# Optimization experiments

Measured on AMD Instinct MI355X. Metric: run time of the kernel, lower is better.

The kernel has to match this reference:

```python
import jax, jax.numpy as jnp
import numpy as np

N, E, FDIM, HID, HEADS, C, L, G = 50000, 800000, 512, 256, 8, 32, 3, 64
EPS = 1e-5


def setup_inputs() -> dict:
    key = jax.random.key(0)
    ks = jax.random.split(key, 16)
    x = jax.random.normal(ks[0], (N, FDIM), dtype=jnp.float32)
    edge_index = jax.random.randint(ks[1], (2, E), 0, N, dtype=jnp.int32)
    batch = jnp.sort(jax.random.randint(ks[2], (N,), 0, G, dtype=jnp.int32))
    s = lambda f: 1.0 / np.sqrt(f)
    return {
        "x": x,
        "edge_index": edge_index,
        "batch": batch,
        "in_w": jax.random.normal(ks[3], (FDIM, HID), jnp.float32) * s(FDIM),
        "in_b": jnp.zeros((HID,), jnp.float32),
        "gat_w": jax.random.normal(ks[4], (L, HID, HID), jnp.float32) * s(HID),
        "att_src": jax.random.normal(ks[5], (L, HEADS, C), jnp.float32) * s(C),
        "att_dst": jax.random.normal(ks[6], (L, HEADS, C), jnp.float32) * s(C),
        "gat_b": jnp.zeros((L, HID), jnp.float32),
        "res_w": jax.random.normal(ks[7], (L, HID, HID), jnp.float32) * s(HID),
        "res_b": jnp.zeros((L, HID), jnp.float32),
        "ln_g": jnp.ones((L, HID), jnp.float32),
        "ln_b": jnp.zeros((L, HID), jnp.float32),
        "pool_w": jax.random.normal(ks[8], (2 * HID, HID), jnp.float32) * s(2 * HID),
        "pool_b": jnp.zeros((HID,), jnp.float32),
    }


def _gat_layer(h, src, dst, w, a_src, a_dst, b):
    # PyG GATConv, concat=True, negative_slope=0.2, dropout inactive (eval)
    xh = (h @ w).reshape(N, HEADS, C)                      # [N,H,C]
    asn = jnp.einsum('nhc,hc->nh', xh, a_src)              # [N,H]
    adn = jnp.einsum('nhc,hc->nh', xh, a_dst)
    e = jax.nn.leaky_relu(asn[src] + adn[dst], 0.2)        # [E2,H]
    # scatter-softmax over destination neighborhoods
    m = jax.ops.segment_max(e, dst, num_segments=N)
    m = jnp.where(jnp.isfinite(m), m, 0.0)
    ex = jnp.exp(e - m[dst])
    den = jax.ops.segment_sum(ex, dst, num_segments=N)
    alpha = ex / (den[dst] + 1e-16)                        # [E2,H]
    msg = xh[src] * alpha[:, :, None]                      # [E2,H,C]
    out = jax.ops.segment_sum(msg, dst, num_segments=N)    # [N,H,C]
    return out.reshape(N, HID) + b


def _layer_norm(h, g, b):
    mu = jnp.mean(h, axis=-1, keepdims=True)
    var = jnp.mean((h - mu) ** 2, axis=-1, keepdims=True)
    return (h - mu) * jax.lax.rsqrt(var + EPS) * g + b


def reference(x, edge_index, batch, in_w, in_b, gat_w, att_src, att_dst, gat_b,
              res_w, res_b, ln_g, ln_b, pool_w, pool_b):
    loops = jnp.arange(N, dtype=edge_index.dtype)          # GATConv add_self_loops=True
    src = jnp.concatenate([edge_index[0], loops])
    dst = jnp.concatenate([edge_index[1], loops])
    h = x @ in_w + in_b
    for i in range(L):
        h_res = h @ res_w[i] + res_b[i]
        h = _gat_layer(h, src, dst, gat_w[i], att_src[i], att_dst[i], gat_b[i])
        h = jax.nn.relu(_layer_norm(h + h_res, ln_g[i], ln_b[i]))
    ones = jnp.ones((N,), h.dtype)
    cnt = jax.ops.segment_sum(ones, batch, num_segments=G)
    h_mean = jax.ops.segment_sum(h, batch, num_segments=G) / jnp.maximum(cnt, 1.0)[:, None]
    h_max = jax.ops.segment_max(h, batch, num_segments=G)
    h_cat = jnp.concatenate([h_mean, h_max], axis=1)       # [G, 2*HID]
    return jax.nn.relu(h_cat @ pool_w + pool_b)            # [G, HID]
```

## Files before the change

kernel.cpp:

```cpp
#include <hip/hip_runtime.h>
#include <math.h>

#define N_NODES 50000
#define E_EDGES 800000
#define E2 (E_EDGES + N_NODES)
#define M_PAD 50048
#define FDIM 512
#define HID 256
#define HEADS 8
#define CDIM 32
#define LAYERS 3
#define GRAPHS 64
#define LN_EPS 1e-5f
#define POOL_P 16

typedef unsigned short ushort_t;
typedef __attribute__((ext_vector_type(8))) short short8v;
typedef __attribute__((ext_vector_type(4))) float f32x4;

__device__ __forceinline__ float bf2f(ushort_t u) {
    union { unsigned int i; float f; } v;
    v.i = ((unsigned int)u) << 16;
    return v.f;
}
__device__ __forceinline__ ushort_t f2bf(float f) {
    union { float f; unsigned int u; } v;
    v.f = f;
    unsigned int r = (v.u + 0x7FFFu + ((v.u >> 16) & 1u)) >> 16;
    return (ushort_t)r;
}
__device__ __forceinline__ void gload_lds16(const void* g, void* l) {
    __builtin_amdgcn_global_load_lds(
        (const __attribute__((address_space(1))) void*)g,
        (__attribute__((address_space(3))) void*)l, 16, 0, 0);
}

__global__ void k_count(const int* __restrict__ ei, int* __restrict__ cnt) {
    int e = blockIdx.x * 256 + threadIdx.x;
    if (e >= E2) return;
    int dst = (e < E_EDGES) ? ei[E_EDGES + e] : (e - E_EDGES);
    atomicAdd(&cnt[dst], 1);
}

__global__ void k_scan1(const int* __restrict__ cnt, int* __restrict__ part) {
    __shared__ int s[256];
    int t = threadIdx.x;
    int i = blockIdx.x * 256 + t;
    s[t] = (i < N_NODES) ? cnt[i] : 0;
    __syncthreads();
    for (int d = 128; d > 0; d >>= 1) {
        if (t < d) s[t] += s[t + d];
        __syncthreads();
    }
    if (t == 0) part[blockIdx.x] = s[0];
}

__global__ void k_scan2(int* __restrict__ part, int nb, int* __restrict__ rowptr) {
    __shared__ int s[256];
    int t = threadIdx.x;
    int v = (t < nb) ? part[t] : 0;
    s[t] = v;
    __syncthreads();
    for (int d = 1; d < 256; d <<= 1) {
        int x = (t >= d) ? s[t - d] : 0;
        __syncthreads();
        s[t] += x;
        __syncthreads();
    }
    if (t < nb) part[t] = s[t] - v;
    if (t == 255) rowptr[N_NODES] = s[255];
}

__global__ void k_scan3(const int* __restrict__ cnt, const int* __restrict__ part,
                        int* __restrict__ rowptr) {
    __shared__ int s[256];
    int t = threadIdx.x;
    int i = blockIdx.x * 256 + t;
    int v = (i < N_NODES) ? cnt[i] : 0;
    s[t] = v;
    __syncthreads();
    for (int d = 1; d < 256; d <<= 1) {
        int x = (t >= d) ? s[t - d] : 0;
        __syncthreads();
        s[t] += x;
        __syncthreads();
    }
    if (i < N_NODES) rowptr[i] = part[blockIdx.x] + s[t] - v;
}

__global__ void k_fill(const int* __restrict__ ei, const int* __restrict__ rowptr,
                       int* __restrict__ fill, int* __restrict__ colv) {
    int e = blockIdx.x * 256 + threadIdx.x;
    if (e >= E2) return;
    int src, dst;
    if (e < E_EDGES) { src = ei[e]; dst = ei[E_EDGES + e]; }
    else             { src = dst = e - E_EDGES; }
    int pos = atomicAdd(&fill[dst], 1);
    colv[rowptr[dst] + pos] = src;
}

__global__ void k_bounds(const int* __restrict__ batch, int* __restrict__ rowstart) {
    int n = blockIdx.x * 256 + threadIdx.x;
    if (n >= N_NODES) return;
    int b = batch[n];
    int bp = (n == 0) ? -1 : batch[n - 1];
    for (int g = bp + 1; g <= b; ++g) rowstart[g] = n;
    if (n == N_NODES - 1) {
        for (int g = b + 1; g <= GRAPHS; ++g) rowstart[g] = N_NODES;
    }
}

__global__ __launch_bounds__(256) void k_cast_x(const float* __restrict__ x,
                                                ushort_t* __restrict__ xb) {
    long long i8 = ((long long)blockIdx.x * 256 + threadIdx.x) * 8;
    if (i8 >= (long long)M_PAD * FDIM) return;
    int row = (int)(i8 >> 9);
    ushort_t o[8];
    if (row < N_NODES) {
        const float* p = x + i8;
        #pragma unroll
        for (int j = 0; j < 8; ++j) o[j] = f2bf(p[j]);
    } else {
        #pragma unroll
        for (int j = 0; j < 8; ++j) o[j] = 0;
    }
    *(short8v*)(xb + i8) = *(short8v*)o;
}

#define MAT_ELEMS (HID * HID)
#define WT_TOTAL (2 * LAYERS * MAT_ELEMS)
__global__ __launch_bounds__(256) void k_wtrans_all(const float* __restrict__ gat_w,
                                                    const float* __restrict__ res_w,
                                                    ushort_t* __restrict__ wt2) {
    int r = blockIdx.x * 256 + threadIdx.x;
    if (r >= WT_TOTAL) return;
    int mat = r >> 16;
    int layer = mat >> 1;
    int isgat = mat & 1;
    int within = r & 65535;
    int k = within >> 8, n = within & 255;
    const float* W = (isgat ? gat_w : res_w) + (size_t)layer * MAT_ELEMS;
    wt2[(size_t)layer * 512 * HID + (size_t)(isgat * 256 + n) * HID + k] =
        f2bf(W[within]);
}

__global__ __launch_bounds__(256) void k_wcomb(const float* __restrict__ in_w,
                                               const ushort_t* __restrict__ wt2_0,
                                               const float* __restrict__ in_b,
                                               const float* __restrict__ res_w0,
                                               const float* __restrict__ gat_w0,
                                               const float* __restrict__ res_b0,
                                               ushort_t* __restrict__ wtC,
                                               float* __restrict__ bC0,
                                               float* __restrict__ bC1) {
    if (blockIdx.x == 512) {
        int n = threadIdx.x;
        float s0 = 0.f, s1 = 0.f;
        for (int k = 0; k < HID; ++k) {
            float ib = in_b[k];
            s0 += ib * res_w0[(size_t)k * HID + n];
            s1 += ib * gat_w0[(size_t)k * HID + n];
        }
        bC0[n] = s0 + res_b0[n];
        bC1[n] = s1;
        return;
    }
    __shared__ float wrow[HID];
    int n = blockIdx.x;
    wrow[threadIdx.x] = bf2f(wt2_0[(size_t)n * HID + threadIdx.x]);
    __syncthreads();
    #pragma unroll
    for (int h = 0; h < 2; ++h) {
        int f = h * 256 + threadIdx.x;
        const float* irow = in_w + (size_t)f * HID;
        float s = 0.f;
        #pragma unroll 4
        for (int k = 0; k < HID; k += 4) {
            float4 iv = *(const float4*)(irow + k);
            s += iv.x * wrow[k] + iv.y * wrow[k + 1]
               + iv.z * wrow[k + 2] + iv.w * wrow[k + 3];
        }
        wtC[(size_t)n * FDIM + f] = f2bf(s);
    }
}

template<int K>
__global__ __launch_bounds__(512) void k_gemm_bf16(const ushort_t* __restrict__ A,
                                                   const ushort_t* __restrict__ BT,
                                                   const float* __restrict__ bias0,
                                                   const float* __restrict__ bias1,
                                                   ushort_t* __restrict__ C0,
                                                   ushort_t* __restrict__ C1,
                                                   const float* __restrict__ a_src,
                                                   const float* __restrict__ a_dst,
                                                   float* __restrict__ asn,
                                                   float* __restrict__ adn, int M) {
    __shared__ char lds[16384] __attribute__((aligned(16)));
    const int bm = blockIdx.x * 128;
    const int bn = blockIdx.y * 128;
    const int t = threadIdx.x, w = t >> 6, l = t & 63;
    const int wr = w & 3, wc = w >> 2;

    const int arow = t >> 2;
    const int aslot = (t & 3) ^ ((arow >> 1) & 3);
    const ushort_t* pa = A + (size_t)(bm + arow) * K + aslot * 8;
    const ushort_t* pb = BT + (size_t)(bn + arow) * K + aslot * 8;
    char* la = lds + w * 1024;
    char* lb = lds + 8192 + w * 1024;

    int aoff[2], boff[4];
    const int kb = l >> 4;
    #pragma unroll
    for (int mi = 0; mi < 2; ++mi) {
        int r = wr * 32 + mi * 16 + (l & 15);
        aoff[mi] = r * 64 + ((kb ^ ((r >> 1) & 3)) << 4);
    }
    #pragma unroll
    for (int ni = 0; ni < 4; ++ni) {
        int c = wc * 64 + ni * 16 + (l & 15);
        boff[ni] = 8192 + c * 64 + ((kb ^ ((c >> 1) & 3)) << 4);
    }

    f32x4 acc[2][4] = {};
    for (int k0 = 0; k0 < K; k0 += 32) {
        gload_lds16(pa + k0, la);
        gload_lds16(pb + k0, lb);
        __syncthreads();
        short8v a[2], b[4];
        #pragma unroll
        for (int mi = 0; mi < 2; ++mi) a[mi] = *(const short8v*)(lds + aoff[mi]);
        #pragma unroll
        for (int ni = 0; ni < 4; ++ni) b[ni] = *(const short8v*)(lds + boff[ni]);
        #pragma unroll
        for (int mi = 0; mi < 2; ++mi)
            #pragma unroll
            for (int ni = 0; ni < 4; ++ni)
                acc[mi][ni] = __builtin_amdgcn_mfma_f32_16x16x32_bf16(
                    a[mi], b[ni], acc[mi][ni], 0, 0, 0);
        __syncthreads();
    }

    ushort_t* C = (bn < 256) ? C0 : C1;
    const float* bias = (bn < 256) ? bias0 : bias1;
    const int cb = (bn < 256) ? bn : bn - 256;
    #pragma unroll
    for (int mi = 0; mi < 2; ++mi) {
        int row = bm + wr * 32 + mi * 16 + (l >> 4) * 4;
        #pragma unroll
        for (int ni = 0; ni < 4; ++ni) {
            int col = cb + wc * 64 + ni * 16 + (l & 15);
            float bv = bias ? bias[col] : 0.f;
            #pragma unroll
            for (int r = 0; r < 4; ++r) {
                if (row + r < M)
                    C[(size_t)(row + r) * HID + col] = f2bf(acc[mi][ni][r] + bv);
            }
        }
    }

    if (asn && bn >= 256) {
        const int cbase = bn - 256;
        #pragma unroll
        for (int mi = 0; mi < 2; ++mi) {
            int row = bm + wr * 32 + mi * 16 + (l >> 4) * 4;
            #pragma unroll
            for (int p = 0; p < 2; ++p) {
                int c0 = cbase + wc * 64 + (2 * p) * 16 + (l & 15);
                int c1c = c0 + 16;
                int head = c0 >> 5;
                float b1a = bias1 ? bias1[c0] : 0.f;
                float b1b = bias1 ? bias1[c1c] : 0.f;
                float as0 = a_src[c0], as1 = a_src[c1c];
                float ad0 = a_dst[c0], ad1 = a_dst[c1c];
                float vs[4], vd[4];
                #pragma unroll
                for (int r = 0; r < 4; ++r) {
                    float x0 = acc[mi][2 * p][r] + b1a;
                    float x1 = acc[mi][2 * p + 1][r] + b1b;
                    vs[r] = x0 * as0 + x1 * as1;
                    vd[r] = x0 * ad0 + x1 * ad1;
                }
                #pragma unroll
                for (int d = 1; d < 16; d <<= 1) {
                    #pragma unroll
                    for (int r = 0; r < 4; ++r) {
                        vs[r] += __shfl_xor(vs[r], d);
                        vd[r] += __shfl_xor(vd[r], d);
                    }
                }
                if ((l & 15) == 0) {
                    #pragma unroll
                    for (int r = 0; r < 4; ++r) {
                        if (row + r < N_NODES) {
                            asn[(row + r) * HEADS + head] = vs[r];
                            adn[(row + r) * HEADS + head] = vd[r];
                        }
                    }
                }
            }
        }
    }
}

__global__ __launch_bounds__(256) void k_agg_ln(const ushort_t* __restrict__ xhb,
                                                const float* __restrict__ asn,
                                                const float* __restrict__ adn,
                                                const int* __restrict__ rowptr,
                                                const int* __restrict__ colv,
                                                const ushort_t* __restrict__ hresb,
                                                const float* __restrict__ gb,
                                                const float* __restrict__ g,
                                                const float* __restrict__ b,
                                                ushort_t* __restrict__ hb) {
    const int wave = threadIdx.x >> 6, lane = threadIdx.x & 63;
    const int n = blockIdx.x * 4 + wave;
    if (n >= N_NODES) return;
    const int half = lane >> 5;
    const int lh = lane & 31;
    const int head = lh >> 2;
    const int ch0 = lh * 8;
    const float adn_h = adn[n * HEADS + head];
    const int j0 = rowptr[n], j1 = rowptr[n + 1];

    float acc[8] = {};
    float den = 0.f;
    int base = j0;
    for (; base + 8 <= j1; base += 8) {
        int idx[4];
        #pragma unroll
        for (int q = 0; q < 4; ++q) idx[q] = colv[base + 2 * q + half];
        short8v u[4];
        #pragma unroll
        for (int q = 0; q < 4; ++q)
            u[q] = *(const short8v*)(xhb + (size_t)idx[q] * HID + ch0);
        float p[4];
        #pragma unroll
        for (int q = 0; q < 4; ++q) {
            float e = asn[idx[q] * HEADS + head] + adn_h;
            e = (e > 0.f) ? e : 0.2f * e;
            p[q] = __expf(e);
        }
        #pragma unroll
        for (int q = 0; q < 4; ++q) {
            den += p[q];
            #pragma unroll
            for (int c = 0; c < 8; ++c)
                acc[c] += p[q] * bf2f((ushort_t)u[q][c]);
        }
    }
    for (; base < j1; base += 2) {
        bool valid = (base + half) < j1;
        int s = valid ? colv[base + half] : n;
        short8v u = *(const short8v*)(xhb + (size_t)s * HID + ch0);
        float e = asn[s * HEADS + head] + adn_h;
        e = (e > 0.f) ? e : 0.2f * e;
        float p = valid ? __expf(e) : 0.f;
        den += p;
        #pragma unroll
        for (int c = 0; c < 8; ++c)
            acc[c] += p * bf2f((ushort_t)u[c]);
    }
    den += __shfl_xor(den, 32);
    #pragma unroll
    for (int c = 0; c < 8; ++c) acc[c] += __shfl_xor(acc[c], 32);

    const float inv = 1.f / (den + 1e-16f);
    short8v hr = *(const short8v*)(hresb + (size_t)n * HID + ch0);
    float4 gbA = *(const float4*)(gb + ch0);
    float4 gbB = *(const float4*)(gb + ch0 + 4);
    float v[8];
    #pragma unroll
    for (int c = 0; c < 8; ++c) {
        float gbv = (c < 4) ? ((const float*)&gbA)[c] : ((const float*)&gbB)[c - 4];
        v[c] = acc[c] * inv + bf2f((ushort_t)hr[c]) + gbv;
    }
    float s = 0.f;
    #pragma unroll
    for (int c = 0; c < 8; ++c) s += v[c];
    #pragma unroll
    for (int d = 1; d < 32; d <<= 1) s += __shfl_xor(s, d);
    const float mu = s * (1.f / HID);
    float q = 0.f;
    #pragma unroll
    for (int c = 0; c < 8; ++c) {
        v[c] -= mu;
        q += v[c] * v[c];
    }
    #pragma unroll
    for (int d = 1; d < 32; d <<= 1) q += __shfl_xor(q, d);
    const float rstd = rsqrtf(q * (1.f / HID) + LN_EPS);
    float4 gA = *(const float4*)(g + ch0);
    float4 gB = *(const float4*)(g + ch0 + 4);
    float4 bA = *(const float4*)(b + ch0);
    float4 bB = *(const float4*)(b + ch0 + 4);
    ushort_t o[8];
    #pragma unroll
    for (int c = 0; c < 8; ++c) {
        float gv = (c < 4) ? ((const float*)&gA)[c] : ((const float*)&gB)[c - 4];
        float bv = (c < 4) ? ((const float*)&bA)[c] : ((const float*)&bB)[c - 4];
        o[c] = f2bf(fmaxf(v[c] * rstd * gv + bv, 0.f));
    }
    if (half == 0)
        *(short8v*)(hb + (size_t)n * HID + ch0) = *(short8v*)o;
}

__global__ __launch_bounds__(256) void k_pool1(const ushort_t* __restrict__ hb,
                                               const int* __restrict__ rowstart,
                                               float* __restrict__ part) {
    int g = blockIdx.x, p = blockIdx.y, c = threadIdx.x;
    int s0 = rowstart[g], s1 = rowstart[g + 1];
    float sum = 0.f, mx = -INFINITY;
    for (int n = s0 + p; n < s1; n += POOL_P) {
        float v = bf2f(hb[(size_t)n * HID + c]);
        sum += v;
        mx = fmaxf(mx, v);
    }
    float* pp = part + (size_t)(g * POOL_P + p) * 512;
    pp[c] = sum;
    pp[256 + c] = mx;
}

__global__ __launch_bounds__(256) void k_pool2g(const float* __restrict__ part,
                                                const int* __restrict__ rowstart,
                                                const float* __restrict__ W,
                                                const float* __restrict__ bias,
                                                float* __restrict__ out) {
    __shared__ float hc[512];
    int g = blockIdx.x, c = threadIdx.x;
    float sum = 0.f, mx = -INFINITY;
    for (int p = 0; p < POOL_P; ++p) {
        const float* pp = part + (size_t)(g * POOL_P + p) * 512;
        sum += pp[c];
        mx = fmaxf(mx, pp[256 + c]);
    }
    float cntf = (float)(rowstart[g + 1] - rowstart[g]);
    hc[c] = sum / fmaxf(cntf, 1.f);
    hc[256 + c] = mx;
    __syncthreads();
    float acc = bias[c];
    #pragma unroll 8
    for (int k = 0; k < 2 * HID; ++k)
        acc += hc[k] * W[(size_t)k * HID + c];
    out[(size_t)g * HID + c] = fmaxf(acc, 0.f);
}

extern "C" void kernel_launch(void* const* d_in, const int* in_sizes, int n_in,
                              void* d_out, int out_size, void* d_ws, size_t ws_size,
                              hipStream_t stream) {
    const float* x       = (const float*)d_in[0];
    const int*   ei      = (const int*)d_in[1];
    const int*   batch   = (const int*)d_in[2];
    const float* in_w    = (const float*)d_in[3];
    const float* in_b    = (const float*)d_in[4];
    const float* gat_w   = (const float*)d_in[5];
    const float* att_src = (const float*)d_in[6];
    const float* att_dst = (const float*)d_in[7];
    const float* gat_b   = (const float*)d_in[8];
    const float* res_w   = (const float*)d_in[9];
    const float* res_b   = (const float*)d_in[10];
    const float* ln_g    = (const float*)d_in[11];
    const float* ln_b    = (const float*)d_in[12];
    const float* pool_w  = (const float*)d_in[13];
    const float* pool_b  = (const float*)d_in[14];
    float* out = (float*)d_out;

    char* ws = (char*)d_ws;
    size_t off = 0;
    auto alloc = [&](size_t bytes) -> char* {
        char* p = ws + off;
        off = (off + bytes + 255) & ~(size_t)255;
        return p;
    };
    ushort_t* xb    = (ushort_t*)alloc((size_t)M_PAD * FDIM * 2);
    ushort_t* hb    = (ushort_t*)alloc((size_t)M_PAD * HID * 2);
    ushort_t* xhb   = (ushort_t*)alloc((size_t)M_PAD * HID * 2);
    ushort_t* hresb = (ushort_t*)alloc((size_t)M_PAD * HID * 2);
    float* asn      = (float*)alloc((size_t)N_NODES * HEADS * 4);
    float* adn      = (float*)alloc((size_t)N_NODES * HEADS * 4);
    int*   cnt      = (int*)alloc((size_t)N_NODES * 4);
    int*   fill     = (int*)alloc((size_t)N_NODES * 4);
    int*   rowptr   = (int*)alloc((size_t)(N_NODES + 1) * 4);
    int*   colv     = (int*)alloc((size_t)E2 * 4);
    int*   part     = (int*)alloc(256 * 4);
    int*   rowstart = (int*)alloc((size_t)(GRAPHS + 1) * 4);
    ushort_t* wt2   = (ushort_t*)alloc((size_t)LAYERS * 512 * HID * 2);
    ushort_t* wtC   = (ushort_t*)alloc((size_t)512 * FDIM * 2);
    float* bC0      = (float*)alloc(HID * 4);
    float* bC1      = (float*)alloc(HID * 4);
    float* poolpart = (float*)alloc((size_t)GRAPHS * POOL_P * 512 * 4);

    hipMemsetAsync(cnt, 0, (size_t)N_NODES * 4, stream);
    hipMemsetAsync(fill, 0, (size_t)N_NODES * 4, stream);

    const int ge = (E2 + 255) / 256;
    const int nb = (N_NODES + 255) / 256;
    k_count<<<ge, 256, 0, stream>>>(ei, cnt);
    k_scan1<<<nb, 256, 0, stream>>>(cnt, part);
    k_scan2<<<1, 256, 0, stream>>>(part, nb, rowptr);
    k_scan3<<<nb, 256, 0, stream>>>(cnt, part, rowptr);
    k_fill<<<ge, 256, 0, stream>>>(ei, rowptr, fill, colv);
    k_bounds<<<nb, 256, 0, stream>>>(batch, rowstart);

    k_cast_x<<<(int)(((size_t)M_PAD * FDIM / 8 + 255) / 256), 256, 0, stream>>>(x, xb);
    k_wtrans_all<<<(WT_TOTAL + 255) / 256, 256, 0, stream>>>(gat_w, res_w, wt2);
    k_wcomb<<<513, 256, 0, stream>>>(in_w, wt2, in_b, res_w, gat_w, res_b,
                                     wtC, bC0, bC1);

    const int nw = (N_NODES + 3) / 4;
    dim3 gg(M_PAD / 128, 4);

    k_gemm_bf16<FDIM><<<gg, 512, 0, stream>>>(xb, wtC, bC0, bC1, hresb, xhb,
                                              att_src, att_dst, asn, adn, N_NODES);
    k_agg_ln<<<nw, 256, 0, stream>>>(xhb, asn, adn, rowptr, colv, hresb,
                                     gat_b, ln_g, ln_b, hb);

    for (int i = 1; i < LAYERS; ++i) {
        k_gemm_bf16<HID><<<gg, 512, 0, stream>>>(hb, wt2 + (size_t)i * 512 * HID,
                                                 res_b + (size_t)i * HID, nullptr,
                                                 hresb, xhb,
                                                 att_src + (size_t)i * HEADS * CDIM,
                                                 att_dst + (size_t)i * HEADS * CDIM,
                                                 asn, adn, N_NODES);
        k_agg_ln<<<nw, 256, 0, stream>>>(xhb, asn, adn, rowptr, colv, hresb,
                                         gat_b + (size_t)i * HID,
                                         ln_g + (size_t)i * HID,
                                         ln_b + (size_t)i * HID, hb);
    }
    dim3 pg(GRAPHS, POOL_P);
    k_pool1<<<pg, 256, 0, stream>>>(hb, rowstart, poolpart);
    k_pool2g<<<GRAPHS, 256, 0, stream>>>(poolpart, rowstart, pool_w, pool_b, out);
}
```

Before: 584.1 us.

## Fuse fp32-to-bf16 input cast into first GEMM and double-buffer LDS tiles

```diff
diff --git a/kernel.cpp b/kernel.cpp
--- a/kernel.cpp
+++ b/kernel.cpp
@@ -108,23 +108,6 @@
     if (n == N_NODES - 1) {
         for (int g = b + 1; g <= GRAPHS; ++g) rowstart[g] = N_NODES;
     }
-}
-
-__global__ __launch_bounds__(256) void k_cast_x(const float* __restrict__ x,
-                                                ushort_t* __restrict__ xb) {
-    long long i8 = ((long long)blockIdx.x * 256 + threadIdx.x) * 8;
-    if (i8 >= (long long)M_PAD * FDIM) return;
-    int row = (int)(i8 >> 9);
-    ushort_t o[8];
-    if (row < N_NODES) {
-        const float* p = x + i8;
-        #pragma unroll
-        for (int j = 0; j < 8; ++j) o[j] = f2bf(p[j]);
-    } else {
-        #pragma unroll
-        for (int j = 0; j < 8; ++j) o[j] = 0;
-    }
-    *(short8v*)(xb + i8) = *(short8v*)o;
 }
 
 #define MAT_ELEMS (HID * HID)
@@ -184,8 +167,8 @@
     }
 }
 
-template<int K>
-__global__ __launch_bounds__(512) void k_gemm_bf16(const ushort_t* __restrict__ A,
+template<int K, bool CVT>
+__global__ __launch_bounds__(512) void k_gemm_bf16(const void* __restrict__ Av,
                                                    const ushort_t* __restrict__ BT,
                                                    const float* __restrict__ bias0,
                                                    const float* __restrict__ bias1,
@@ -195,7 +178,8 @@
                                                    const float* __restrict__ a_dst,
                                                    float* __restrict__ asn,
                                                    float* __restrict__ adn, int M) {
-    __shared__ char lds[16384] __attribute__((aligned(16)));
+    __shared__ char lds[32768] __attribute__((aligned(16)));
+    constexpr int NT = K / 32;
     const int bm = blockIdx.x * 128;
     const int bn = blockIdx.y * 128;
     const int t = threadIdx.x, w = t >> 6, l = t & 63;
@@ -203,10 +187,12 @@
 
     const int arow = t >> 2;
     const int aslot = (t & 3) ^ ((arow >> 1) & 3);
-    const ushort_t* pa = A + (size_t)(bm + arow) * K + aslot * 8;
+    int growA = bm + arow;
+    if (CVT && growA >= M) growA = 0;
+    const float*    pax = CVT ? (const float*)Av + (size_t)growA * K + aslot * 8 : nullptr;
+    const ushort_t* pa  = CVT ? nullptr
+                              : (const ushort_t*)Av + (size_t)growA * K + aslot * 8;
     const ushort_t* pb = BT + (size_t)(bn + arow) * K + aslot * 8;
-    char* la = lds + w * 1024;
-    char* lb = lds + 8192 + w * 1024;
 
     int aoff[2], boff[4];
     const int kb = l >> 4;
@@ -221,16 +207,34 @@
         boff[ni] = 8192 + c * 64 + ((kb ^ ((c >> 1) & 3)) << 4);
     }
 
+    auto STAGE = [&](int bufsel, int k0) {
+        char* base = lds + bufsel * 16384;
+        if constexpr (CVT) {
+            const float* s = pax + k0;
+            float4 v0 = *(const float4*)(s);
+            float4 v1 = *(const float4*)(s + 4);
+            ushort_t o[8];
+            o[0] = f2bf(v0.x); o[1] = f2bf(v0.y); o[2] = f2bf(v0.z); o[3] = f2bf(v0.w);
+            o[4] = f2bf(v1.x); o[5] = f2bf(v1.y); o[6] = f2bf(v1.z); o[7] = f2bf(v1.w);
+            *(short8v*)(base + t * 16) = *(short8v*)o;
+        } else {
+            gload_lds16(pa + k0, base + w * 1024);
+        }
+        gload_lds16(pb + k0, base + 8192 + w * 1024);
+    };
+
+    STAGE(0, 0);
+    __syncthreads();
+
     f32x4 acc[2][4] = {};
-    for (int k0 = 0; k0 < K; k0 += 32) {
-        gload_lds16(pa + k0, la);
-        gload_lds16(pb + k0, lb);
-        __syncthreads();
+    for (int tt = 0; tt < NT; ++tt) {
+        if (tt + 1 < NT) STAGE((tt + 1) & 1, (tt + 1) * 32);
+        const char* base = lds + (tt & 1) * 16384;
         short8v a[2], b[4];
         #pragma unroll
-        for (int mi = 0; mi < 2; ++mi) a[mi] = *(const short8v*)(lds + aoff[mi]);
-        #pragma unroll
-        for (int ni = 0; ni < 4; ++ni) b[ni] = *(const short8v*)(lds + boff[ni]);
+        for (int mi = 0; mi < 2; ++mi) a[mi] = *(const short8v*)(base + aoff[mi]);
+        #pragma unroll
+        for (int ni = 0; ni < 4; ++ni) b[ni] = *(const short8v*)(base + boff[ni]);
         #pragma unroll
         for (int mi = 0; mi < 2; ++mi)
             #pragma unroll
@@ -471,7 +475,6 @@
         off = (off + bytes + 255) & ~(size_t)255;
         return p;
     };
-    ushort_t* xb    = (ushort_t*)alloc((size_t)M_PAD * FDIM * 2);
     ushort_t* hb    = (ushort_t*)alloc((size_t)M_PAD * HID * 2);
     ushort_t* xhb   = (ushort_t*)alloc((size_t)M_PAD * HID * 2);
     ushort_t* hresb = (ushort_t*)alloc((size_t)M_PAD * HID * 2);
@@ -501,7 +504,6 @@
     k_fill<<<ge, 256, 0, stream>>>(ei, rowptr, fill, colv);
     k_bounds<<<nb, 256, 0, stream>>>(batch, rowstart);
 
-    k_cast_x<<<(int)(((size_t)M_PAD * FDIM / 8 + 255) / 256), 256, 0, stream>>>(x, xb);
     k_wtrans_all<<<(WT_TOTAL + 255) / 256, 256, 0, stream>>>(gat_w, res_w, wt2);
     k_wcomb<<<513, 256, 0, stream>>>(in_w, wt2, in_b, res_w, gat_w, res_b,
                                      wtC, bC0, bC1);
@@ -509,18 +511,18 @@
     const int nw = (N_NODES + 3) / 4;
     dim3 gg(M_PAD / 128, 4);
 
-    k_gemm_bf16<FDIM><<<gg, 512, 0, stream>>>(xb, wtC, bC0, bC1, hresb, xhb,
-                                              att_src, att_dst, asn, adn, N_NODES);
+    k_gemm_bf16<FDIM, true><<<gg, 512, 0, stream>>>((const void*)x, wtC, bC0, bC1,
+                                                    hresb, xhb, att_src, att_dst,
+                                                    asn, adn, N_NODES);
     k_agg_ln<<<nw, 256, 0, stream>>>(xhb, asn, adn, rowptr, colv, hresb,
                                      gat_b, ln_g, ln_b, hb);
 
     for (int i = 1; i < LAYERS; ++i) {
-        k_gemm_bf16<HID><<<gg, 512, 0, stream>>>(hb, wt2 + (size_t)i * 512 * HID,
-                                                 res_b + (size_t)i * HID, nullptr,
-                                                 hresb, xhb,
-                                                 att_src + (size_t)i * HEADS * CDIM,
-                                                 att_dst + (size_t)i * HEADS * CDIM,
-                                                 asn, adn, N_NODES);
+        k_gemm_bf16<HID, false><<<gg, 512, 0, stream>>>(
+            (const void*)hb, wt2 + (size_t)i * 512 * HID,
+            res_b + (size_t)i * HID, nullptr, hresb, xhb,
+            att_src + (size_t)i * HEADS * CDIM,
+            att_dst + (size_t)i * HEADS * CDIM, asn, adn, N_NODES);
         k_agg_ln<<<nw, 256, 0, stream>>>(xhb, asn, adn, rowptr, colv, hresb,
                                          gat_b + (size_t)i * HID,
                                          ln_g + (size_t)i * HID,
```

Measured after the change: 590.5 us. About the same (+1.1%).
